# Performance work log

Measured on AMD Instinct MI355X. Metric: run time of the kernel, lower is better.

The kernel has to match this reference:

```python
import jax, jax.numpy as jnp
import numpy as np

B, CIN, T = 64, 64, 4096
F, K = 128, 64


def setup_inputs() -> dict:
    key = jax.random.key(0)
    k1, k2, k3, k4, k5 = jax.random.split(key, 5)
    x = jax.random.normal(k1, (B, CIN, T), dtype=jnp.float32)
    conv_weights = jax.random.normal(k2, (F, K), dtype=jnp.float32) * 0.2
    spat_weights = jax.random.normal(k3, (F, CIN), dtype=jnp.float32) * 0.2
    weight = jax.random.normal(k4, (F,), dtype=jnp.float32)
    bias = jax.random.normal(k5, (F,), dtype=jnp.float32)
    return {"x": x, "conv_weights": conv_weights, "spat_weights": spat_weights,
            "weight": weight, "bias": bias}


def reference(x, conv_weights, spat_weights, weight, bias):
    n_filters, ksize = conv_weights.shape
    n_in = spat_weights.shape[1]
    # rank-1 merged kernel: [F, Cin, K]
    merged = conv_weights[:, None, :] * spat_weights[:, :, None]
    # valid conv1d: x [B,Cin,T] -> conved [B,F,T-K+1]
    conved = jax.lax.conv_general_dilated(
        x, merged, window_strides=(1,), padding='VALID',
        dimension_numbers=('NCH', 'OIH', 'NCH'))
    # per-filter weight norm
    norm_w = jnp.sqrt(jnp.sum(merged * merged, axis=(1, 2)))  # [F]
    # input norm: sliding-window sum of x^2 over channels and window
    sq = jnp.sum(x * x, axis=1, keepdims=True)  # [B,1,T]
    ones_k = jnp.ones((1, 1, ksize), dtype=x.dtype)
    slide = jax.lax.conv_general_dilated(
        sq, ones_k, window_strides=(1,), padding='VALID',
        dimension_numbers=('NCH', 'OIH', 'NCH'))[:, 0, :]  # [B,Tout]
    norm_inputs = jnp.sqrt(slide)
    scale = np.sqrt(n_in * ksize).astype(np.float32)
    cos_sims = conved / (norm_w[None, :, None] * norm_inputs[:, None, :]) * scale
    mean_cos = jnp.mean(jnp.abs(cos_sims), axis=2)  # [B,F]
    out_per_wave = mean_cos * weight[None, :] + bias[None, :]
    return jnp.sum(out_per_wave, axis=1)  # [B]
```

## Files before the change

### kernel.cpp

```cpp
#include <hip/hip_runtime.h>
#include <hip/hip_bf16.h>
#include <cstdint>
#include <cstddef>

#define BB   64
#define CINN 64
#define TS   4096
#define FF   128
#define KS   64
#define TOUT (TS - KS + 1)
#define TT   2048
#define FGZ  8
#define SEG  (TT + KS)

#define TPB   256
#define SXT   37
#define SYB   68

typedef __attribute__((ext_vector_type(8))) short short8;
typedef __attribute__((ext_vector_type(4))) float f32x4;
union FragU { unsigned int u[4]; short8 v; uint4 q4; };

static __device__ __forceinline__ unsigned int f2bf_u(float f) {
    __hip_bfloat16 h = __float2bfloat16(f);
    return (unsigned int)*reinterpret_cast<unsigned short*>(&h);
}

__global__ void k_band(const float* __restrict__ cw, const float* __restrict__ sw,
                       const float* __restrict__ weight,
                       uint4* __restrict__ bandB, float* __restrict__ wnf) {
    const int f = blockIdx.x, l = threadIdx.x;
    const int n = l & 15, q = l >> 4;
    for (int s = 0; s < 3; ++s) {
        FragU o;
#pragma unroll
        for (int i = 0; i < 4; ++i) {
            int i0 = 32 * s + 8 * q + 2 * i - n;
            int i1 = i0 + 1;
            float a = (i0 >= 0 && i0 < KS) ? cw[(size_t)f * KS + i0] : 0.f;
            float c = (i1 >= 0 && i1 < KS) ? cw[(size_t)f * KS + i1] : 0.f;
            o.u[i] = f2bf_u(a) | (f2bf_u(c) << 16);
        }
        bandB[((size_t)f * 3 + s) * 64 + l] = o.q4;
    }
    float a = sw[(size_t)f * CINN + l], c = cw[(size_t)f * KS + l];
    float v = a * a, u = c * c;
    for (int off = 32; off > 0; off >>= 1) {
        v += __shfl_down(v, off, 64);
        u += __shfl_down(u, off, 64);
    }
    if (l == 0) wnf[f] = weight[f] * rsqrtf(v * u) * (64.0f / (float)TOUT);
}

__global__ __launch_bounds__(256) void k_spatial_mfma(
    const float* __restrict__ x, const float* __restrict__ sw,
    __hip_bfloat16* __restrict__ y, float* __restrict__ sq)
{
    __shared__ unsigned int xTd[TPB * SXT];
    __shared__ float ybuf[4 * 32 * SYB];
    __shared__ float sqred[4 * TPB];
    const int tid = threadIdx.x;
    const int b = blockIdx.y;
    const int t0 = blockIdx.x * TPB;

    {
        const int tj = tid & 63;
        const int cg = tid >> 6;
        float4 s4 = {0.f, 0.f, 0.f, 0.f};
#pragma unroll
        for (int i = 0; i < 8; ++i) {
            int cp = cg * 8 + i;
            const float* xr = x + ((size_t)b * CINN + 2 * cp) * TS + t0 + 4 * tj;
            float4 v0 = *(const float4*)xr;
            float4 v1 = *(const float4*)(xr + TS);
            s4.x += v0.x * v0.x + v1.x * v1.x;
            s4.y += v0.y * v0.y + v1.y * v1.y;
            s4.z += v0.z * v0.z + v1.z * v1.z;
            s4.w += v0.w * v0.w + v1.w * v1.w;
            xTd[(4 * tj + 0) * SXT + cp] = f2bf_u(v0.x) | (f2bf_u(v1.x) << 16);
            xTd[(4 * tj + 1) * SXT + cp] = f2bf_u(v0.y) | (f2bf_u(v1.y) << 16);
            xTd[(4 * tj + 2) * SXT + cp] = f2bf_u(v0.z) | (f2bf_u(v1.z) << 16);
            xTd[(4 * tj + 3) * SXT + cp] = f2bf_u(v0.w) | (f2bf_u(v1.w) << 16);
        }
        *(float4*)(sqred + cg * TPB + 4 * tj) = s4;
    }
    __syncthreads();
    if (tid < 64) {
        float4 a0 = *(const float4*)(sqred + 4 * tid);
        float4 a1 = *(const float4*)(sqred + TPB + 4 * tid);
        float4 a2 = *(const float4*)(sqred + 2 * TPB + 4 * tid);
        float4 a3 = *(const float4*)(sqred + 3 * TPB + 4 * tid);
        float4 s; s.x = a0.x + a1.x + a2.x + a3.x; s.y = a0.y + a1.y + a2.y + a3.y;
        s.z = a0.z + a1.z + a2.z + a3.z; s.w = a0.w + a1.w + a2.w + a3.w;
        *(float4*)(sq + (size_t)b * TS + t0 + 4 * tid) = s;
    }

    const int w  = tid >> 6;
    const int ln = tid & 63;
    const int m  = ln & 15;
    const int q  = ln >> 4;
    const int fbase = 32 * w;

    short8 Afr[2][2];
#pragma unroll
    for (int p = 0; p < 2; ++p)
#pragma unroll
        for (int s = 0; s < 2; ++s) {
            const float* swr = sw + (size_t)(fbase + 16 * p + m) * CINN + s * 32 + q * 8;
            float4 w0 = *(const float4*)swr;
            float4 w1 = *(const float4*)(swr + 4);
            FragU fa;
            fa.u[0] = f2bf_u(w0.x) | (f2bf_u(w0.y) << 16);
            fa.u[1] = f2bf_u(w0.z) | (f2bf_u(w0.w) << 16);
            fa.u[2] = f2bf_u(w1.x) | (f2bf_u(w1.y) << 16);
            fa.u[3] = f2bf_u(w1.z) | (f2bf_u(w1.w) << 16);
            Afr[p][s] = fa.v;
        }

    const int baseB = m * SXT + q * 4;
    float* yb = ybuf + w * (32 * SYB);

#pragma unroll
    for (int strip = 0; strip < 4; ++strip) {
#pragma unroll
        for (int tti = 0; tti < 4; ++tti) {
            const int tt = strip * 4 + tti;
            const int ad = baseB + tt * (16 * SXT);
            FragU b0, b1;
#pragma unroll
            for (int i = 0; i < 4; ++i) { b0.u[i] = xTd[ad + i]; b1.u[i] = xTd[ad + 16 + i]; }
            f32x4 acc0 = {0.f, 0.f, 0.f, 0.f};
            f32x4 acc1 = {0.f, 0.f, 0.f, 0.f};
            acc0 = __builtin_amdgcn_mfma_f32_16x16x32_bf16(Afr[0][0], b0.v, acc0, 0, 0, 0);
            acc0 = __builtin_amdgcn_mfma_f32_16x16x32_bf16(Afr[0][1], b1.v, acc0, 0, 0, 0);
            acc1 = __builtin_amdgcn_mfma_f32_16x16x32_bf16(Afr[1][0], b0.v, acc1, 0, 0, 0);
            acc1 = __builtin_amdgcn_mfma_f32_16x16x32_bf16(Afr[1][1], b1.v, acc1, 0, 0, 0);
            const int tl = tti * 16 + m;
#pragma unroll
            for (int r = 0; r < 4; ++r) {
                yb[(4 * q + r) * SYB + tl]      = acc0[r];
                yb[(16 + 4 * q + r) * SYB + tl] = acc1[r];
            }
        }
#pragma unroll
        for (int pr = 0; pr < 8; ++pr) {
            const int fl = pr * 4 + q;
            float4 v = *(const float4*)(yb + fl * SYB + 4 * m);
            uint2 o;
            o.x = f2bf_u(v.x) | (f2bf_u(v.y) << 16);
            o.y = f2bf_u(v.z) | (f2bf_u(v.w) << 16);
            *(uint2*)(y + ((size_t)b * FF + fbase + fl) * TS + t0 + strip * 64 + 4 * m) = o;
        }
    }
}

__global__ __launch_bounds__(256) void k_temporal_direct(
    const __hip_bfloat16* __restrict__ y, const float* __restrict__ sq,
    const uint4* __restrict__ bandB, const float* __restrict__ wnf,
    const float* __restrict__ bias, float* __restrict__ out)
{
    __shared__ float rbuf[SEG];
    __shared__ float wred[4];
    const int tid = threadIdx.x;
    const int ln = tid & 63, w = tid >> 6;
    const int m = ln & 15, q = ln >> 4;
    const int b = blockIdx.y;
    const int t0 = blockIdx.x * TT;
    const int f0 = blockIdx.z * FGZ;

    const float* sqrow = sq + (size_t)b * TS;
#pragma unroll
    for (int it = 0; it < 3; ++it) {
        int j = tid + 256 * it;
        if (j < SEG / 4) {
            int p = t0 + 4 * j; if (p > TS - 4) p = TS - 4;
            *(float4*)(rbuf + 4 * j) = *(const float4*)(sqrow + p);
        }
    }
    __syncthreads();

    const int base = 8 * tid;
    float rv[8];
    {
        float hd[8], tl[8];
        float s = 0.f;
#pragma unroll
        for (int mm = 0; mm < 16; ++mm) {
            float4 v = *(const float4*)(rbuf + base + 4 * mm);
            if (mm < 2) { hd[4 * mm] = v.x; hd[4 * mm + 1] = v.y; hd[4 * mm + 2] = v.z; hd[4 * mm + 3] = v.w; }
            s += (v.x + v.y) + (v.z + v.w);
        }
        float4 ta = *(const float4*)(rbuf + base + 64);
        float4 tb = *(const float4*)(rbuf + base + 68);
        tl[0] = ta.x; tl[1] = ta.y; tl[2] = ta.z; tl[3] = ta.w;
        tl[4] = tb.x; tl[5] = tb.y; tl[6] = tb.z; tl[7] = tb.w;
#pragma unroll
        for (int j = 0; j < 8; ++j) {
            int tpos = t0 + base + j;
            rv[j] = (tpos < TOUT) ? rsqrtf(s) : 0.f;
            s += tl[j] - hd[j];
        }
    }
    __syncthreads();
#pragma unroll
    for (int j = 0; j < 8; ++j) {
        int tl = base + j;
        int nn = tl & 15, mr = (tl >> 4) & 15, tile = tl >> 8;
        rbuf[tile * 256 + ((mr >> 2) * 16 + nn) * 4 + (mr & 3)] = rv[j];
    }
    __syncthreads();

    const __hip_bfloat16* ybase = y + ((size_t)b * FF + f0) * TS + t0 + 16 * m + 8 * q;
    float acc = 0.f;
    for (int fi = 0; fi < FGZ; ++fi) {
        const uint4* bb = bandB + (size_t)(f0 + fi) * 3 * 64;
        FragU B0, B1, B2;
        B0.q4 = bb[ln]; B1.q4 = bb[64 + ln]; B2.q4 = bb[128 + ln];
        const __hip_bfloat16* yr = ybase + (size_t)fi * TS;
        float facc = 0.f;
#pragma unroll
        for (int ti = 0; ti < 2; ++ti) {
            const int tile = 2 * w + ti;
            FragU a0, a1, a2;
            a0.q4 = *(const uint4*)(yr + tile * 256);
            a1.q4 = *(const uint4*)(yr + tile * 256 + 32);
            a2.q4 = *(const uint4*)(yr + tile * 256 + 64);
            f32x4 d = {0.f, 0.f, 0.f, 0.f};
            d = __builtin_amdgcn_mfma_f32_16x16x32_bf16(a0.v, B0.v, d, 0, 0, 0);
            d = __builtin_amdgcn_mfma_f32_16x16x32_bf16(a1.v, B1.v, d, 0, 0, 0);
            d = __builtin_amdgcn_mfma_f32_16x16x32_bf16(a2.v, B2.v, d, 0, 0, 0);
            float4 r4 = *(const float4*)(rbuf + tile * 256 + 4 * ln);
            float rr[4]; *(float4*)rr = r4;
#pragma unroll
            for (int r = 0; r < 4; ++r) facc += fabsf(d[r]) * rr[r];
        }
        acc += wnf[f0 + fi] * facc;
    }

    for (int off = 32; off > 0; off >>= 1) acc += __shfl_down(acc, off, 64);
    if (ln == 0) wred[w] = acc;
    __syncthreads();
    if (tid == 0) atomicAdd(out + b, wred[0] + wred[1] + wred[2] + wred[3]);
    if (blockIdx.x == 0 && blockIdx.z == 0 && tid < FF) {
        float v = bias[tid];
        for (int off = 32; off > 0; off >>= 1) v += __shfl_down(v, off, 64);
        if ((tid & 63) == 0) atomicAdd(out + b, v);
    }
}

__global__ __launch_bounds__(256) void k_naive(
    const float* __restrict__ x, const float* __restrict__ cw,
    const float* __restrict__ sw, const float* __restrict__ weight,
    const float* __restrict__ bias, float* __restrict__ out)
{
    __shared__ float yl[TS];
    __shared__ float ql[TS];
    __shared__ float wred[4];
    const int f = blockIdx.x, b = blockIdx.y, tid = threadIdx.x;
    for (int t = tid; t < TS; t += 256) {
        float a = 0.f, s = 0.f;
        for (int c = 0; c < CINN; ++c) {
            float v = x[((size_t)b * CINN + c) * TS + t];
            a += sw[(size_t)f * CINN + c] * v;
            s += v * v;
        }
        yl[t] = a; ql[t] = s;
    }
    __syncthreads();
    float acc = 0.f;
    for (int t = tid; t < TOUT; t += 256) {
        float cv = 0.f, sl = 0.f;
        for (int k = 0; k < KS; ++k) { cv += cw[(size_t)f * KS + k] * yl[t + k]; sl += ql[t + k]; }
        acc += fabsf(cv) * rsqrtf(sl);
    }
    float ssw = 0.f, scw = 0.f;
    for (int c = 0; c < CINN; ++c) { float v = sw[(size_t)f * CINN + c]; ssw += v * v; }
    for (int k = 0; k < KS; ++k)   { float v = cw[(size_t)f * KS + k];  scw += v * v; }
    const float wnf = weight[f] * rsqrtf(ssw * scw) * 64.0f / (float)TOUT;
    for (int off = 32; off > 0; off >>= 1) acc += __shfl_down(acc, off, 64);
    if ((tid & 63) == 0) wred[tid >> 6] = acc;
    __syncthreads();
    if (tid == 0) {
        float tot = (wred[0] + wred[1] + wred[2] + wred[3]) * wnf;
        if (f == 0) {
            float bsum = 0.f;
            for (int ff = 0; ff < FF; ++ff) bsum += bias[ff];
            tot += bsum;
        }
        atomicAdd(out + b, tot);
    }
}

extern "C" void kernel_launch(void* const* d_in, const int* in_sizes, int n_in,
                              void* d_out, int out_size, void* d_ws, size_t ws_size,
                              hipStream_t stream) {
    const float* x  = (const float*)d_in[0];
    const float* cw = (const float*)d_in[1];
    const float* sw = (const float*)d_in[2];
    const float* w  = (const float*)d_in[3];
    const float* bs = (const float*)d_in[4];
    float* out = (float*)d_out;

    hipMemsetAsync(d_out, 0, (size_t)out_size * sizeof(float), stream);

    const size_t yBytes    = (size_t)BB * FF * TS * sizeof(__hip_bfloat16);
    const size_t padBytes  = 4096;
    const size_t sqBytes   = (size_t)BB * TS * sizeof(float);
    const size_t bandBytes = (size_t)FF * 3 * 64 * 16;
    const size_t wnBytes   = (size_t)FF * sizeof(float);

    if (yBytes + padBytes + sqBytes + bandBytes + wnBytes <= ws_size) {
        __hip_bfloat16* ybf = (__hip_bfloat16*)d_ws;
        char* p = (char*)d_ws + yBytes;
        hipMemsetAsync(p, 0, padBytes, stream);
        float* sq    = (float*)(p + padBytes);
        uint4* bandB = (uint4*)(p + padBytes + sqBytes);
        float* wnf   = (float*)(p + padBytes + sqBytes + bandBytes);
        k_band<<<dim3(FF), 64, 0, stream>>>(cw, sw, w, bandB, wnf);
        k_spatial_mfma  <<<dim3(TS / TPB, BB), 256, 0, stream>>>(x, sw, ybf, sq);
        k_temporal_direct<<<dim3(TS / TT, BB, FF / FGZ), 256, 0, stream>>>(ybf, sq, bandB, wnf, bs, out);
    } else {
        k_naive<<<dim3(FF, BB), 256, 0, stream>>>(x, cw, sw, w, bs, out);
    }
}
```

Measured before the change: 142.2 us.

## Fuse spatial and temporal stages into one kernel keeping intermediate in LDS

Merges the spatial MFMA projection and the temporal banded MFMA convolution into a single 1024-thread kernel per (time segment, batch). The bf16 intermediate and the squared-norm sliding window now stay in shared memory, with a 64-sample halo recomputed per segment. This removes the global write and re-read of the large B×F×T bf16 intermediate and the sq buffer, and drops a kernel launch. In exchange the kernel uses a lot of LDS per block, which lowers occupancy, and the halo adds some redundant spatial compute.

```diff
diff --git a/kernel.cpp b/kernel.cpp
--- a/kernel.cpp
+++ b/kernel.cpp
@@ -9,13 +9,12 @@
 #define FF   128
 #define KS   64
 #define TOUT (TS - KS + 1)
-#define TT   2048
-#define FGZ  8
-#define SEG  (TT + KS)
-
-#define TPB   256
-#define SXT   37
-#define SYB   68
+
+#define TSEG 256
+#define XROW 320
+#define SXTW 35
+#define YW   336
+#define YWW  (YW / 2)
 
 typedef __attribute__((ext_vector_type(8))) short short8;
 typedef __attribute__((ext_vector_type(4))) float f32x4;
@@ -52,61 +51,104 @@
     if (l == 0) wnf[f] = weight[f] * rsqrtf(v * u) * (64.0f / (float)TOUT);
 }
 
-__global__ __launch_bounds__(256) void k_spatial_mfma(
+__global__ __launch_bounds__(1024, 4) void k_fused(
     const float* __restrict__ x, const float* __restrict__ sw,
-    __hip_bfloat16* __restrict__ y, float* __restrict__ sq)
+    const uint4* __restrict__ bandB, const float* __restrict__ wnf,
+    const float* __restrict__ bias, float* __restrict__ out)
 {
-    __shared__ unsigned int xTd[TPB * SXT];
-    __shared__ float ybuf[4 * 32 * SYB];
-    __shared__ float sqred[4 * TPB];
+    __shared__ unsigned int xT[XROW * SXTW];
+    __shared__ unsigned int yL[FF * YWW];
+    __shared__ float wred[16];
+
     const int tid = threadIdx.x;
+    const int w = tid >> 6, l = tid & 63;
     const int b = blockIdx.y;
-    const int t0 = blockIdx.x * TPB;
+    const int t0 = blockIdx.x * TSEG;
 
     {
-        const int tj = tid & 63;
-        const int cg = tid >> 6;
-        float4 s4 = {0.f, 0.f, 0.f, 0.f};
-#pragma unroll
-        for (int i = 0; i < 8; ++i) {
-            int cp = cg * 8 + i;
-            const float* xr = x + ((size_t)b * CINN + 2 * cp) * TS + t0 + 4 * tj;
-            float4 v0 = *(const float4*)xr;
-            float4 v1 = *(const float4*)(xr + TS);
-            s4.x += v0.x * v0.x + v1.x * v1.x;
-            s4.y += v0.y * v0.y + v1.y * v1.y;
-            s4.z += v0.z * v0.z + v1.z * v1.z;
-            s4.w += v0.w * v0.w + v1.w * v1.w;
-            xTd[(4 * tj + 0) * SXT + cp] = f2bf_u(v0.x) | (f2bf_u(v1.x) << 16);
-            xTd[(4 * tj + 1) * SXT + cp] = f2bf_u(v0.y) | (f2bf_u(v1.y) << 16);
-            xTd[(4 * tj + 2) * SXT + cp] = f2bf_u(v0.z) | (f2bf_u(v1.z) << 16);
-            xTd[(4 * tj + 3) * SXT + cp] = f2bf_u(v0.w) | (f2bf_u(v1.w) << 16);
-        }
-        *(float4*)(sqred + cg * TPB + 4 * tj) = s4;
-    }
-    __syncthreads();
-    if (tid < 64) {
-        float4 a0 = *(const float4*)(sqred + 4 * tid);
-        float4 a1 = *(const float4*)(sqred + TPB + 4 * tid);
-        float4 a2 = *(const float4*)(sqred + 2 * TPB + 4 * tid);
-        float4 a3 = *(const float4*)(sqred + 3 * TPB + 4 * tid);
-        float4 s; s.x = a0.x + a1.x + a2.x + a3.x; s.y = a0.y + a1.y + a2.y + a3.y;
-        s.z = a0.z + a1.z + a2.z + a3.z; s.w = a0.w + a1.w + a2.w + a3.w;
-        *(float4*)(sq + (size_t)b * TS + t0 + 4 * tid) = s;
-    }
-
-    const int w  = tid >> 6;
-    const int ln = tid & 63;
-    const int m  = ln & 15;
-    const int q  = ln >> 4;
-    const int fbase = 32 * w;
-
-    short8 Afr[2][2];
-#pragma unroll
-    for (int p = 0; p < 2; ++p)
+        const float* xb = x + (size_t)b * CINN * TS;
+        float* sqp = (float*)yL;
+        float4 s4a = {0.f, 0.f, 0.f, 0.f}, s4b = {0.f, 0.f, 0.f, 0.f};
+#pragma unroll
+        for (int r = 0; r < 2; ++r) {
+            const int cp = w + 16 * r;
+            const float* x0 = xb + (size_t)(2 * cp) * TS;
+            {
+                int p = t0 + 4 * l; if (p > TS - 4) p = TS - 4;
+                float4 v0 = *(const float4*)(x0 + p);
+                float4 v1 = *(const float4*)(x0 + TS + p);
+                s4a.x += v0.x * v0.x + v1.x * v1.x;
+                s4a.y += v0.y * v0.y + v1.y * v1.y;
+                s4a.z += v0.z * v0.z + v1.z * v1.z;
+                s4a.w += v0.w * v0.w + v1.w * v1.w;
+                const int t = 4 * l;
+                xT[(t + 0) * SXTW + cp] = f2bf_u(v0.x) | (f2bf_u(v1.x) << 16);
+                xT[(t + 1) * SXTW + cp] = f2bf_u(v0.y) | (f2bf_u(v1.y) << 16);
+                xT[(t + 2) * SXTW + cp] = f2bf_u(v0.z) | (f2bf_u(v1.z) << 16);
+                xT[(t + 3) * SXTW + cp] = f2bf_u(v0.w) | (f2bf_u(v1.w) << 16);
+            }
+            if (l < 16) {
+                int p = t0 + 256 + 4 * l; if (p > TS - 4) p = TS - 4;
+                float4 v0 = *(const float4*)(x0 + p);
+                float4 v1 = *(const float4*)(x0 + TS + p);
+                s4b.x += v0.x * v0.x + v1.x * v1.x;
+                s4b.y += v0.y * v0.y + v1.y * v1.y;
+                s4b.z += v0.z * v0.z + v1.z * v1.z;
+                s4b.w += v0.w * v0.w + v1.w * v1.w;
+                const int t = 256 + 4 * l;
+                xT[(t + 0) * SXTW + cp] = f2bf_u(v0.x) | (f2bf_u(v1.x) << 16);
+                xT[(t + 1) * SXTW + cp] = f2bf_u(v0.y) | (f2bf_u(v1.y) << 16);
+                xT[(t + 2) * SXTW + cp] = f2bf_u(v0.z) | (f2bf_u(v1.z) << 16);
+                xT[(t + 3) * SXTW + cp] = f2bf_u(v0.w) | (f2bf_u(v1.w) << 16);
+            }
+        }
+        *(float4*)(sqp + w * XROW + 4 * l) = s4a;
+        if (l < 16) *(float4*)(sqp + w * XROW + 256 + 4 * l) = s4b;
+    }
+    __syncthreads();
+
+    if (tid < XROW) {
+        const float* sqp = (const float*)yL;
+        float s = 0.f;
+#pragma unroll
+        for (int w2 = 0; w2 < 16; ++w2) s += sqp[w2 * XROW + tid];
+        xT[tid * SXTW + 32] = __float_as_uint(s);
+    }
+    __syncthreads();
+
+    const int m = l & 15, q = l >> 4;
+
+    if (w == 0 && l < 32) {
+        const int base = 8 * l;
+        float s = 0.f, hd[8], tl[8];
+#pragma unroll
+        for (int k = 0; k < 64; ++k) {
+            float v = __uint_as_float(xT[(base + k) * SXTW + 32]);
+            if (k < 8) hd[k] = v;
+            s += v;
+        }
+#pragma unroll
+        for (int j = 0; j < 8; ++j) tl[j] = __uint_as_float(xT[(base + 64 + j) * SXTW + 32]);
+        float rv[8];
+#pragma unroll
+        for (int j = 0; j < 8; ++j) {
+            int tpos = t0 + base + j;
+            rv[j] = (tpos < TOUT) ? rsqrtf(s) : 0.f;
+            s += tl[j] - hd[j];
+        }
+#pragma unroll
+        for (int j = 0; j < 8; ++j) {
+            int t = base + j;
+            xT[t * SXTW + 32 + ((t >> 6) & 1)] = __float_as_uint(rv[j]);
+        }
+    }
+
+    {
+        const int mw = w & 7, nh = w >> 3;
+        short8 Af[2];
 #pragma unroll
         for (int s = 0; s < 2; ++s) {
-            const float* swr = sw + (size_t)(fbase + 16 * p + m) * CINN + s * 32 + q * 8;
+            const float* swr = sw + (size_t)(16 * mw + m) * CINN + s * 32 + q * 8;
             float4 w0 = *(const float4*)swr;
             float4 w1 = *(const float4*)(swr + 4);
             FragU fa;
@@ -114,134 +156,80 @@
             fa.u[1] = f2bf_u(w0.z) | (f2bf_u(w0.w) << 16);
             fa.u[2] = f2bf_u(w1.x) | (f2bf_u(w1.y) << 16);
             fa.u[3] = f2bf_u(w1.z) | (f2bf_u(w1.w) << 16);
-            Afr[p][s] = fa.v;
-        }
-
-    const int baseB = m * SXT + q * 4;
-    float* yb = ybuf + w * (32 * SYB);
-
-#pragma unroll
-    for (int strip = 0; strip < 4; ++strip) {
-#pragma unroll
-        for (int tti = 0; tti < 4; ++tti) {
-            const int tt = strip * 4 + tti;
-            const int ad = baseB + tt * (16 * SXT);
+            Af[s] = fa.v;
+        }
+        const bool evenl = (l & 1) == 0;
+#pragma unroll
+        for (int ti = 0; ti < 10; ++ti) {
+            const int tt = nh * 10 + ti;
+            const int t = tt * 16 + m;
+            const int bw = t * SXTW + 4 * q;
             FragU b0, b1;
 #pragma unroll
-            for (int i = 0; i < 4; ++i) { b0.u[i] = xTd[ad + i]; b1.u[i] = xTd[ad + 16 + i]; }
-            f32x4 acc0 = {0.f, 0.f, 0.f, 0.f};
-            f32x4 acc1 = {0.f, 0.f, 0.f, 0.f};
-            acc0 = __builtin_amdgcn_mfma_f32_16x16x32_bf16(Afr[0][0], b0.v, acc0, 0, 0, 0);
-            acc0 = __builtin_amdgcn_mfma_f32_16x16x32_bf16(Afr[0][1], b1.v, acc0, 0, 0, 0);
-            acc1 = __builtin_amdgcn_mfma_f32_16x16x32_bf16(Afr[1][0], b0.v, acc1, 0, 0, 0);
-            acc1 = __builtin_amdgcn_mfma_f32_16x16x32_bf16(Afr[1][1], b1.v, acc1, 0, 0, 0);
-            const int tl = tti * 16 + m;
+            for (int i = 0; i < 4; ++i) { b0.u[i] = xT[bw + i]; b1.u[i] = xT[bw + 16 + i]; }
+            f32x4 acc = {0.f, 0.f, 0.f, 0.f};
+            acc = __builtin_amdgcn_mfma_f32_16x16x32_bf16(Af[0], b0.v, acc, 0, 0, 0);
+            acc = __builtin_amdgcn_mfma_f32_16x16x32_bf16(Af[1], b1.v, acc, 0, 0, 0);
 #pragma unroll
             for (int r = 0; r < 4; ++r) {
-                yb[(4 * q + r) * SYB + tl]      = acc0[r];
-                yb[(16 + 4 * q + r) * SYB + tl] = acc1[r];
+                float o = __shfl_xor(acc[r], 1, 64);
+                if (evenl) {
+                    unsigned u = f2bf_u(acc[r]) | (f2bf_u(o) << 16);
+                    yL[(16 * mw + 4 * q + r) * YWW + 8 * tt + (m >> 1)] = u;
+                }
             }
         }
-#pragma unroll
-        for (int pr = 0; pr < 8; ++pr) {
-            const int fl = pr * 4 + q;
-            float4 v = *(const float4*)(yb + fl * SYB + 4 * m);
-            uint2 o;
-            o.x = f2bf_u(v.x) | (f2bf_u(v.y) << 16);
-            o.y = f2bf_u(v.z) | (f2bf_u(v.w) << 16);
-            *(uint2*)(y + ((size_t)b * FF + fbase + fl) * TS + t0 + strip * 64 + 4 * m) = o;
-        }
-    }
-}
-
-__global__ __launch_bounds__(256) void k_temporal_direct(
-    const __hip_bfloat16* __restrict__ y, const float* __restrict__ sq,
-    const uint4* __restrict__ bandB, const float* __restrict__ wnf,
-    const float* __restrict__ bias, float* __restrict__ out)
-{
-    __shared__ float rbuf[SEG];
-    __shared__ float wred[4];
-    const int tid = threadIdx.x;
-    const int ln = tid & 63, w = tid >> 6;
-    const int m = ln & 15, q = ln >> 4;
-    const int b = blockIdx.y;
-    const int t0 = blockIdx.x * TT;
-    const int f0 = blockIdx.z * FGZ;
-
-    const float* sqrow = sq + (size_t)b * TS;
-#pragma unroll
-    for (int it = 0; it < 3; ++it) {
-        int j = tid + 256 * it;
-        if (j < SEG / 4) {
-            int p = t0 + 4 * j; if (p > TS - 4) p = TS - 4;
-            *(float4*)(rbuf + 4 * j) = *(const float4*)(sqrow + p);
-        }
-    }
-    __syncthreads();
-
-    const int base = 8 * tid;
-    float rv[8];
+        yL[(tid >> 3) * YWW + 160 + (tid & 7)] = 0u;
+    }
+    __syncthreads();
+
+    float rr[4];
+#pragma unroll
+    for (int r = 0; r < 4; ++r) {
+        int t = 64 * q + 16 * r + m;
+        rr[r] = __uint_as_float(xT[t * SXTW + 32 + (q & 1)]);
+    }
+    const int f0t = 8 * w;
+    float acc = 0.f;
+    uint4 pb0, pb1, pb2;
     {
-        float hd[8], tl[8];
+        const uint4* bb = bandB + (size_t)f0t * 3 * 64;
+        pb0 = bb[l]; pb1 = bb[64 + l]; pb2 = bb[128 + l];
+    }
+#pragma unroll 2
+    for (int fi = 0; fi < 8; ++fi) {
+        const int f = f0t + fi;
+        FragU B0, B1, B2;
+        B0.q4 = pb0; B1.q4 = pb1; B2.q4 = pb2;
+        if (fi < 7) {
+            const uint4* bb = bandB + (size_t)(f + 1) * 3 * 64;
+            pb0 = bb[l]; pb1 = bb[64 + l]; pb2 = bb[128 + l];
+        }
+        const int abase = f * YWW + 8 * m + 4 * q;
+        FragU a0, a1, a2;
+        a0.q4 = *(const uint4*)(yL + abase);
+        a1.q4 = *(const uint4*)(yL + abase + 16);
+        a2.q4 = *(const uint4*)(yL + abase + 32);
+        f32x4 d = {0.f, 0.f, 0.f, 0.f};
+        d = __builtin_amdgcn_mfma_f32_16x16x32_bf16(a0.v, B0.v, d, 0, 0, 0);
+        d = __builtin_amdgcn_mfma_f32_16x16x32_bf16(a1.v, B1.v, d, 0, 0, 0);
+        d = __builtin_amdgcn_mfma_f32_16x16x32_bf16(a2.v, B2.v, d, 0, 0, 0);
+        float facc = 0.f;
+#pragma unroll
+        for (int r = 0; r < 4; ++r) facc += fabsf(d[r]) * rr[r];
+        acc += wnf[f] * facc;
+    }
+
+    for (int off = 32; off > 0; off >>= 1) acc += __shfl_down(acc, off, 64);
+    if (l == 0) wred[w] = acc;
+    __syncthreads();
+    if (tid == 0) {
         float s = 0.f;
 #pragma unroll
-        for (int mm = 0; mm < 16; ++mm) {
-            float4 v = *(const float4*)(rbuf + base + 4 * mm);
-            if (mm < 2) { hd[4 * mm] = v.x; hd[4 * mm + 1] = v.y; hd[4 * mm + 2] = v.z; hd[4 * mm + 3] = v.w; }
-            s += (v.x + v.y) + (v.z + v.w);
-        }
-        float4 ta = *(const float4*)(rbuf + base + 64);
-        float4 tb = *(const float4*)(rbuf + base + 68);
-        tl[0] = ta.x; tl[1] = ta.y; tl[2] = ta.z; tl[3] = ta.w;
-        tl[4] = tb.x; tl[5] = tb.y; tl[6] = tb.z; tl[7] = tb.w;
-#pragma unroll
-        for (int j = 0; j < 8; ++j) {
-            int tpos = t0 + base + j;
-            rv[j] = (tpos < TOUT) ? rsqrtf(s) : 0.f;
-            s += tl[j] - hd[j];
-        }
-    }
-    __syncthreads();
-#pragma unroll
-    for (int j = 0; j < 8; ++j) {
-        int tl = base + j;
-        int nn = tl & 15, mr = (tl >> 4) & 15, tile = tl >> 8;
-        rbuf[tile * 256 + ((mr >> 2) * 16 + nn) * 4 + (mr & 3)] = rv[j];
-    }
-    __syncthreads();
-
-    const __hip_bfloat16* ybase = y + ((size_t)b * FF + f0) * TS + t0 + 16 * m + 8 * q;
-    float acc = 0.f;
-    for (int fi = 0; fi < FGZ; ++fi) {
-        const uint4* bb = bandB + (size_t)(f0 + fi) * 3 * 64;
-        FragU B0, B1, B2;
-        B0.q4 = bb[ln]; B1.q4 = bb[64 + ln]; B2.q4 = bb[128 + ln];
-        const __hip_bfloat16* yr = ybase + (size_t)fi * TS;
-        float facc = 0.f;
-#pragma unroll
-        for (int ti = 0; ti < 2; ++ti) {
-            const int tile = 2 * w + ti;
-            FragU a0, a1, a2;
-            a0.q4 = *(const uint4*)(yr + tile * 256);
-            a1.q4 = *(const uint4*)(yr + tile * 256 + 32);
-            a2.q4 = *(const uint4*)(yr + tile * 256 + 64);
-            f32x4 d = {0.f, 0.f, 0.f, 0.f};
-            d = __builtin_amdgcn_mfma_f32_16x16x32_bf16(a0.v, B0.v, d, 0, 0, 0);
-            d = __builtin_amdgcn_mfma_f32_16x16x32_bf16(a1.v, B1.v, d, 0, 0, 0);
-            d = __builtin_amdgcn_mfma_f32_16x16x32_bf16(a2.v, B2.v, d, 0, 0, 0);
-            float4 r4 = *(const float4*)(rbuf + tile * 256 + 4 * ln);
-            float rr[4]; *(float4*)rr = r4;
-#pragma unroll
-            for (int r = 0; r < 4; ++r) facc += fabsf(d[r]) * rr[r];
-        }
-        acc += wnf[f0 + fi] * facc;
-    }
-
-    for (int off = 32; off > 0; off >>= 1) acc += __shfl_down(acc, off, 64);
-    if (ln == 0) wred[w] = acc;
-    __syncthreads();
-    if (tid == 0) atomicAdd(out + b, wred[0] + wred[1] + wred[2] + wred[3]);
-    if (blockIdx.x == 0 && blockIdx.z == 0 && tid < FF) {
+        for (int i = 0; i < 16; ++i) s += wred[i];
+        atomicAdd(out + b, s);
+    }
+    if (blockIdx.x == 0 && tid < FF) {
         float v = bias[tid];
         for (int off = 32; off > 0; off >>= 1) v += __shfl_down(v, off, 64);
         if ((tid & 63) == 0) atomicAdd(out + b, v);
@@ -303,22 +291,14 @@
 
     hipMemsetAsync(d_out, 0, (size_t)out_size * sizeof(float), stream);
 
-    const size_t yBytes    = (size_t)BB * FF * TS * sizeof(__hip_bfloat16);
-    const size_t padBytes  = 4096;
-    const size_t sqBytes   = (size_t)BB * TS * sizeof(float);
     const size_t bandBytes = (size_t)FF * 3 * 64 * 16;
     const size_t wnBytes   = (size_t)FF * sizeof(float);
 
-    if (yBytes + padBytes + sqBytes + bandBytes + wnBytes <= ws_size) {
-        __hip_bfloat16* ybf = (__hip_bfloat16*)d_ws;
-        char* p = (char*)d_ws + yBytes;
-        hipMemsetAsync(p, 0, padBytes, stream);
-        float* sq    = (float*)(p + padBytes);
-        uint4* bandB = (uint4*)(p + padBytes + sqBytes);
-        float* wnf   = (float*)(p + padBytes + sqBytes + bandBytes);
-        k_band<<<dim3(FF), 64, 0, stream>>>(cw, sw, w, bandB, wnf);
-        k_spatial_mfma  <<<dim3(TS / TPB, BB), 256, 0, stream>>>(x, sw, ybf, sq);
-        k_temporal_direct<<<dim3(TS / TT, BB, FF / FGZ), 256, 0, stream>>>(ybf, sq, bandB, wnf, bs, out);
+    if (bandBytes + wnBytes <= ws_size) {
+        uint4* bandB = (uint4*)d_ws;
+        float* wnf   = (float*)((char*)d_ws + bandBytes);
+        k_band <<<dim3(FF), 64, 0, stream>>>(cw, sw, w, bandB, wnf);
+        k_fused<<<dim3(TS / TSEG, BB), 1024, 0, stream>>>(x, sw, bandB, wnf, bs, out);
     } else {
         k_naive<<<dim3(FF, BB), 256, 0, stream>>>(x, cw, sw, w, bs, out);
     }
```

Measured after the change: 151.0 us. 6.2% more time.
